# Kernel optimization log

Hardware: AMD Instinct MI355X
Metric: run time of the kernel (lower is better)

Reference implementation:

```python
import jax, jax.numpy as jnp
import numpy as np

N, E, B, C, L, HLS = 30000, 480000, 64, 128, 3, 64
PARAM_NAMES = ['Wq','bq','Wk','bk','Wv','bv','Wskip','bskip','lstm_Wih_f','lstm_Whh_f','lstm_bih_f','lstm_bhh_f','lstm_Wih_b','lstm_Whh_b','lstm_bih_b','lstm_bhh_b','att_W','att_b','gP_W1','gP_b1','gP_W2','gP_b2','gT_W1','gT_b1','gT_W2','gT_b2','m_W0','m_b0','m_W1','m_b1','m_W2','m_b2']


def setup_inputs() -> dict:
    key = jax.random.key(0)
    ks = iter(jax.random.split(key, 64))
    rn = lambda shape: jax.random.normal(next(ks), shape, dtype=jnp.float32) * 0.05
    inp = {
        'x': jax.random.normal(next(ks), (N, C), dtype=jnp.float32),
        'edge_index': jax.random.randint(next(ks), (2, E), 0, N, dtype=jnp.int32),
        'batch': jnp.sort(jax.random.randint(next(ks), (N,), 0, B, dtype=jnp.int32)),
        'hls_attr': jax.random.normal(next(ks), (B, HLS), dtype=jnp.float32),
        'Wq': rn((L, C, C)), 'bq': rn((L, C)),
        'Wk': rn((L, C, C)), 'bk': rn((L, C)),
        'Wv': rn((L, C, C)), 'bv': rn((L, C)),
        'Wskip': rn((L, C, C)), 'bskip': rn((L, C)),
        'lstm_Wih_f': rn((4 * C, C)), 'lstm_Whh_f': rn((4 * C, C)),
        'lstm_bih_f': rn((4 * C,)), 'lstm_bhh_f': rn((4 * C,)),
        'lstm_Wih_b': rn((4 * C, C)), 'lstm_Whh_b': rn((4 * C, C)),
        'lstm_bih_b': rn((4 * C,)), 'lstm_bhh_b': rn((4 * C,)),
        'att_W': rn((2 * C, 1)), 'att_b': rn((1,)),
        'gP_W1': rn((C, C)), 'gP_b1': rn((C,)), 'gP_W2': rn((C, 1)), 'gP_b2': rn((1,)),
        'gT_W1': rn((C, C)), 'gT_b1': rn((C,)), 'gT_W2': rn((C, 1)), 'gT_b2': rn((1,)),
        'm_W0': rn((2 * C + HLS, 64)), 'm_b0': rn((64,)),
        'm_W1': rn((64, 64)), 'm_b1': rn((64,)),
        'm_W2': rn((64, 1)), 'm_b2': rn((1,)),
    }
    return inp


def _segment_softmax(logits, seg, num):
    m = jax.ops.segment_max(logits, seg, num_segments=num)
    e = jnp.exp(logits - m[seg])
    d = jax.ops.segment_sum(e, seg, num_segments=num)
    return e / d[seg]


def _lstm(xs, Wih, Whh, bih, bhh):
    # xs: [L, N, C] -> outputs [L, N, H]
    H = Whh.shape[1]
    h0 = jnp.zeros((xs.shape[1], H), xs.dtype)
    bias = bih + bhh
    def step(carry, xt):
        h, c = carry
        z = xt @ Wih.T + h @ Whh.T + bias
        i, f, g, o = jnp.split(z, 4, axis=-1)
        c = jax.nn.sigmoid(f) * c + jax.nn.sigmoid(i) * jnp.tanh(g)
        h = jax.nn.sigmoid(o) * jnp.tanh(c)
        return (h, c), h
    _, hs = jax.lax.scan(step, (h0, h0), xs)
    return hs


def _gate_pool(x, batch, W1, b1, W2, b2):
    gate = jax.nn.relu(x @ W1 + b1) @ W2 + b2          # [N, 1]
    gate = _segment_softmax(gate[:, 0], batch, B)[:, None]
    return jax.ops.segment_sum(gate * x, batch, num_segments=B)


def _forward(x, edge_index, batch, hls_attr, Wq, bq, Wk, bk, Wv, bv, Wskip, bskip,
             lstm_Wih_f, lstm_Whh_f, lstm_bih_f, lstm_bhh_f,
             lstm_Wih_b, lstm_Whh_b, lstm_bih_b, lstm_bhh_b,
             att_W, att_b, gP_W1, gP_b1, gP_W2, gP_b2, gT_W1, gT_b1, gT_W2, gT_b2,
             m_W0, m_b0, m_W1, m_b1, m_W2, m_b2):
    src, dst = edge_index[0], edge_index[1]
    scale = 1.0 / jnp.sqrt(jnp.asarray(C, jnp.float32))
    h_list = []
    for i in range(L):
        q = x @ Wq[i] + bq[i]
        k = x @ Wk[i] + bk[i]
        v = x @ Wv[i] + bv[i]
        logits = jnp.sum(q[dst] * k[src], axis=-1) * scale   # [E]
        alpha = _segment_softmax(logits, dst, N)             # per-dst softmax
        agg = jax.ops.segment_sum(alpha[:, None] * v[src], dst, num_segments=N)
        x = jax.nn.relu(agg + x @ Wskip[i] + bskip[i])       # TransformerConv + root skip, then ReLU
        h_list.append(x)
    xs = jnp.stack(h_list)                                   # [L, N, C]
    hf = _lstm(xs, lstm_Wih_f, lstm_Whh_f, lstm_bih_f, lstm_bhh_f)
    hb = _lstm(xs[::-1], lstm_Wih_b, lstm_Whh_b, lstm_bih_b, lstm_bhh_b)[::-1]
    hcat = jnp.concatenate([hf, hb], axis=-1)                # [L, N, 2C]
    a = jax.nn.softmax((hcat @ att_W)[..., 0] + att_b[0], axis=0)  # softmax over layers
    x = jnp.sum(a[..., None] * xs, axis=0)                   # [N, C] JK-LSTM output
    out_P = _gate_pool(x, batch, gP_W1, gP_b1, gP_W2, gP_b2)
    out_T = _gate_pool(x, batch, gT_W1, gT_b1, gT_W2, gT_b2)
    h = jnp.concatenate([out_P, out_T, hls_attr], axis=-1)   # [B, 2C+HLS]
    h = jax.nn.relu(h @ m_W0 + m_b0)
    h = jax.nn.relu(h @ m_W1 + m_b1)
    return h @ m_W2 + m_b2                                   # [B, 1]


def reference(x, edge_index, batch, hls_attr, Wq, bq, Wk, bk, Wv, bv, Wskip, bskip,
              lstm_Wih_f, lstm_Whh_f, lstm_bih_f, lstm_bhh_f,
              lstm_Wih_b, lstm_Whh_b, lstm_bih_b, lstm_bhh_b,
              att_W, att_b, gP_W1, gP_b1, gP_W2, gP_b2, gT_W1, gT_b1, gT_W2, gT_b2,
              m_W0, m_b0, m_W1, m_b1, m_W2, m_b2):
    return _forward(x, edge_index, batch, hls_attr, Wq, bq, Wk, bk, Wv, bv, Wskip, bskip,
                    lstm_Wih_f, lstm_Whh_f, lstm_bih_f, lstm_bhh_f,
                    lstm_Wih_b, lstm_Whh_b, lstm_bih_b, lstm_bhh_b,
                    att_W, att_b, gP_W1, gP_b1, gP_W2, gP_b2, gT_W1, gT_b1, gT_W2, gT_b2,
                    m_W0, m_b0, m_W1, m_b1, m_W2, m_b2)
```

## Files before the change

### kernel.cpp

```cpp
#include <hip/hip_runtime.h>
#include <math.h>

#define NN 30000
#define EE 480000
#define BB 64
#define CC 128
#define LLAYERS 3
#define HLSD 64

typedef __attribute__((ext_vector_type(8))) short bf16x8;
typedef __attribute__((ext_vector_type(4))) float f32x4;

__device__ inline unsigned short f2bf(float f){
  unsigned u = __float_as_uint(f);
  u += 0x7fffu + ((u >> 16) & 1u);
  return (unsigned short)(u >> 16);
}
__device__ inline float bf2f(unsigned short h){
  return __uint_as_float(((unsigned)h) << 16);
}

__global__ void k_hist(const int* __restrict__ dst, int* __restrict__ counts, int E){
  int e = blockIdx.x*256 + threadIdx.x;
  if (e < E) atomicAdd(&counts[dst[e]], 1);
}
__global__ void k_scan_block(const int* __restrict__ counts, int* __restrict__ row_ptr,
                             int* __restrict__ bsums, int n){
  __shared__ int sm[256];
  int i = blockIdx.x*256 + threadIdx.x;
  int v = (i < n) ? counts[i] : 0;
  sm[threadIdx.x] = v; __syncthreads();
  for (int off = 1; off < 256; off <<= 1){
    int t = (threadIdx.x >= off) ? sm[threadIdx.x - off] : 0;
    __syncthreads();
    sm[threadIdx.x] += t;
    __syncthreads();
  }
  if (i < n) row_ptr[i+1] = sm[threadIdx.x];
  if (threadIdx.x == 255) bsums[blockIdx.x] = sm[255];
}
__global__ void k_scan_bsums(const int* __restrict__ bsums, int* __restrict__ bexcl, int nb){
  if (threadIdx.x == 0 && blockIdx.x == 0){
    int s = 0;
    for (int i = 0; i < nb; i++){ int t = bsums[i]; bexcl[i] = s; s += t; }
  }
}
__global__ void k_scan_add(int* __restrict__ row_ptr, const int* __restrict__ bexcl, int n){
  int i = blockIdx.x*256 + threadIdx.x;
  if (i < n) row_ptr[i+1] += bexcl[i >> 8];
  if (i == 0) row_ptr[0] = 0;
}
__global__ void k_fill(const int* __restrict__ src, const int* __restrict__ dst,
                       const int* __restrict__ row_ptr, int* __restrict__ fill,
                       int* __restrict__ esrc, int E){
  int e = blockIdx.x*256 + threadIdx.x;
  if (e < E){
    int d = dst[e];
    int pos = row_ptr[d] + atomicAdd(&fill[d], 1);
    esrc[pos] = src[e];
  }
}

struct PrepPtrs {
  const float* tsrc[14]; unsigned short* tdst[14];
  const float* csrc[4];  unsigned short* cdst[4];
  const float *bihf, *bhhf, *bihb, *bhhb;
  float *cbf, *cbb;
};
__global__ __launch_bounds__(256) void k_prep(PrepPtrs p){
  int b = blockIdx.x, tid = threadIdx.x;
  if (b < 14){
    const float* s = p.tsrc[b]; unsigned short* d = p.tdst[b];
    for (int i = tid; i < 16384; i += 256){
      int k = i >> 7, n = i & 127;
      d[n*128 + k] = f2bf(s[i]);
    }
  } else if (b < 30){
    int m = (b - 14) >> 2, ch = (b - 14) & 3;
    const float* s = p.csrc[m] + ch*16384; unsigned short* d = p.cdst[m] + ch*16384;
    for (int i = tid; i < 16384; i += 256) d[i] = f2bf(s[i]);
  } else {
    for (int i = tid; i < 512; i += 256){
      p.cbf[i] = p.bihf[i] + p.bhhf[i];
      p.cbb[i] = p.bihb[i] + p.bhhb[i];
    }
  }
}
__global__ __launch_bounds__(256) void k_cvt_x(const float* __restrict__ src,
                                               unsigned short* __restrict__ dst, int n8){
  int i = blockIdx.x*256 + threadIdx.x;
  if (i >= n8) return;
  float4 a = *(const float4*)(src + (size_t)i*8);
  float4 b = *(const float4*)(src + (size_t)i*8 + 4);
  union { unsigned short u[8]; uint4 v; } o;
  o.u[0]=f2bf(a.x); o.u[1]=f2bf(a.y); o.u[2]=f2bf(a.z); o.u[3]=f2bf(a.w);
  o.u[4]=f2bf(b.x); o.u[5]=f2bf(b.y); o.u[6]=f2bf(b.z); o.u[7]=f2bf(b.w);
  *(uint4*)(dst + (size_t)i*8) = o.v;
}

struct Quad { const unsigned short* Bt[4]; const float* bias[4]; };

template<int RELU, int OUTBF16>
__global__ __launch_bounds__(256) void k_mfma_gemm(
    const unsigned short* __restrict__ A0, Quad qd,
    float* __restrict__ Cf, unsigned short* __restrict__ Cb,
    int M, int ldC, int colsPerMat)
{
  __shared__ unsigned short As0[64*128];
  __shared__ unsigned short Bs0[64*128];

  const int tid = threadIdx.x;
  const int row0 = blockIdx.x*64;
  const int colg0 = blockIdx.y*64;
  const int mi = colg0 / colsPerMat;
  const int nloc = colg0 - mi*colsPerMat;
  const unsigned short* Bt0 = qd.Bt[mi];

  #pragma unroll
  for (int i = 0; i < 4; i++){
    int ch = tid + i*256;
    int r = ch >> 4, c16 = ch & 15;
    int gr = row0 + r;
    uint4 av = make_uint4(0,0,0,0);
    if (gr < M) av = *(const uint4*)(A0 + (size_t)gr*128 + c16*8);
    *(uint4*)((char*)As0 + ((r*256 + c16*16) ^ ((r&7)<<4))) = av;
    uint4 bv = *(const uint4*)(Bt0 + (size_t)(nloc + r)*128 + c16*8);
    *(uint4*)((char*)Bs0 + ((r*256 + c16*16) ^ ((r&7)<<4))) = bv;
  }
  __syncthreads();

  const int w = tid >> 6, l = tid & 63;
  const int lr = l & 15, lhi = l >> 4;

  f32x4 acc[4];
  #pragma unroll
  for (int f = 0; f < 4; f++){ acc[f][0]=0.f; acc[f][1]=0.f; acc[f][2]=0.f; acc[f][3]=0.f; }

  #pragma unroll
  for (int kt = 0; kt < 4; kt++){
    int arow = w*16 + lr;
    bf16x8 a = *(const bf16x8*)((const char*)As0 + ((arow*256 + kt*64 + lhi*16) ^ ((arow&7)<<4)));
    #pragma unroll
    for (int f = 0; f < 4; f++){
      int brow = f*16 + lr;
      bf16x8 b = *(const bf16x8*)((const char*)Bs0 + ((brow*256 + kt*64 + lhi*16) ^ ((brow&7)<<4)));
      acc[f] = __builtin_amdgcn_mfma_f32_16x16x32_bf16(a, b, acc[f], 0, 0, 0);
    }
  }

  const float* bias = qd.bias[mi];
  #pragma unroll
  for (int f = 0; f < 4; f++){
    int colg = colg0 + f*16 + lr;
    float bv = bias ? bias[nloc + f*16 + lr] : 0.f;
    #pragma unroll
    for (int r = 0; r < 4; r++){
      int grow = row0 + w*16 + lhi*4 + r;
      if (grow < M){
        float v = acc[f][r] + bv;
        if (RELU) v = fmaxf(v, 0.f);
        if (OUTBF16) Cb[(size_t)grow*ldC + colg] = f2bf(v);
        else         Cf[(size_t)grow*ldC + colg] = v;
      }
    }
  }
}

template<int FIRST>
__global__ __launch_bounds__(256) void k_lstm_fused(
    const unsigned short* __restrict__ X,
    const unsigned short* __restrict__ H,
    const unsigned short* __restrict__ Wih,
    const unsigned short* __restrict__ Whh,
    const float* __restrict__ cbias,
    unsigned short* __restrict__ Hout,
    float* __restrict__ Cst,
    float* __restrict__ score,
    const float* __restrict__ attW,
    int M)
{
  __shared__ unsigned short As[64*128];
  __shared__ unsigned short Bs[128*128];
  const int tid = threadIdx.x;
  const int row0 = blockIdx.x*64;
  const int t0 = blockIdx.y*32;
  const int w = tid >> 6, l = tid & 63, lr = l & 15, lhi = l >> 4;

  f32x4 acc[8];
  #pragma unroll
  for (int f = 0; f < 8; f++){ acc[f][0]=0.f; acc[f][1]=0.f; acc[f][2]=0.f; acc[f][3]=0.f; }

  const int npair = FIRST ? 1 : 2;
  for (int pair = 0; pair < npair; pair++){
    const unsigned short* A  = pair ? H   : X;
    const unsigned short* Bt = pair ? Whh : Wih;
    if (pair) __syncthreads();
    #pragma unroll
    for (int i = 0; i < 4; i++){
      int ch = tid + i*256;
      int r = ch >> 4, c16 = ch & 15;
      int gr = row0 + r;
      uint4 av = make_uint4(0,0,0,0);
      if (gr < M) av = *(const uint4*)(A + (size_t)gr*128 + c16*8);
      *(uint4*)((char*)As + ((r*256 + c16*16) ^ ((r&7)<<4))) = av;
    }
    #pragma unroll
    for (int i = 0; i < 8; i++){
      int ch = tid + i*256;
      int r = ch >> 4, c16 = ch & 15;
      int gr = (r >> 5)*128 + t0 + (r & 31);
      uint4 bv = *(const uint4*)(Bt + (size_t)gr*128 + c16*8);
      *(uint4*)((char*)Bs + ((r*256 + c16*16) ^ ((r&7)<<4))) = bv;
    }
    __syncthreads();
    #pragma unroll
    for (int kt = 0; kt < 4; kt++){
      int arow = w*16 + lr;
      bf16x8 a = *(const bf16x8*)((const char*)As + ((arow*256 + kt*64 + lhi*16) ^ ((arow&7)<<4)));
      #pragma unroll
      for (int f = 0; f < 8; f++){
        int brow = f*16 + lr;
        bf16x8 b = *(const bf16x8*)((const char*)Bs + ((brow*256 + kt*64 + lhi*16) ^ ((brow&7)<<4)));
        acc[f] = __builtin_amdgcn_mfma_f32_16x16x32_bf16(a, b, acc[f], 0, 0, 0);
      }
    }
  }

  float sc[4] = {0.f, 0.f, 0.f, 0.f};
  #pragma unroll
  for (int cb = 0; cb < 2; cb++){
    int t = t0 + cb*16 + lr;
    float aw  = attW[t];
    float bi  = cbias[t];
    float bf_ = cbias[128 + t];
    float bg  = cbias[256 + t];
    float bo  = cbias[384 + t];
    #pragma unroll
    for (int r = 0; r < 4; r++){
      int grow = row0 + w*16 + lhi*4 + r;
      if (grow < M){
        float zi = acc[0+cb][r] + bi;
        float zf = acc[2+cb][r] + bf_;
        float zg = acc[4+cb][r] + bg;
        float zo = acc[6+cb][r] + bo;
        float cp = FIRST ? 0.f : Cst[(size_t)grow*128 + t];
        float si = 1.f/(1.f + expf(-zi));
        float sf = 1.f/(1.f + expf(-zf));
        float so = 1.f/(1.f + expf(-zo));
        float cn = sf*cp + si*tanhf(zg);
        float hn = so*tanhf(cn);
        Cst[(size_t)grow*128 + t] = cn;
        Hout[(size_t)grow*128 + t] = f2bf(hn);
        sc[r] += hn * aw;
      }
    }
  }
  #pragma unroll
  for (int r = 0; r < 4; r++){
    float p = sc[r];
    p += __shfl_xor(p, 1, 64);
    p += __shfl_xor(p, 2, 64);
    p += __shfl_xor(p, 4, 64);
    p += __shfl_xor(p, 8, 64);
    if (lr == 0){
      int grow = row0 + w*16 + lhi*4 + r;
      if (grow < M) atomicAdd(&score[grow], p);
    }
  }
}

__global__ __launch_bounds__(256) void k_attn(
    const unsigned short* __restrict__ qkvs, const int* __restrict__ row_ptr,
    const int* __restrict__ esrc, unsigned short* __restrict__ xout, int n)
{
  int wid = threadIdx.x >> 6, lane = threadIdx.x & 63;
  int dst = blockIdx.x*4 + wid;
  if (dst >= n) return;
  const int g = lane >> 4, j = lane & 15;
  const size_t drow = (size_t)dst*512;

  bf16x8 qv = *(const bf16x8*)(qkvs + drow + j*8);
  float qf[8];
  #pragma unroll
  for (int i = 0; i < 8; i++) qf[i] = bf2f((unsigned short)qv[i]);

  const int rs = row_ptr[dst], re = row_ptr[dst+1];
  const float scale2 = 0.08838834764831845f * 1.4426950408889634f;
  float m = -INFINITY, den = 0.f;
  float acc[8];
  #pragma unroll
  for (int i = 0; i < 8; i++) acc[i] = 0.f;

  int e = rs + g;
  if (e < re){
    int s = esrc[e];
    const unsigned short* sr = qkvs + (size_t)s*512 + j*8;
    bf16x8 kc = *(const bf16x8*)(sr + 128);
    bf16x8 vc = *(const bf16x8*)(sr + 256);
    while (true){
      int en = e + 4;
      bool havenext = en < re;
      bf16x8 kn, vn;
      if (havenext){
        int sn = esrc[en];
        const unsigned short* srn = qkvs + (size_t)sn*512 + j*8;
        kn = *(const bf16x8*)(srn + 128);
        vn = *(const bf16x8*)(srn + 256);
      }
      float d = qf[0]*bf2f((unsigned short)kc[0]);
      #pragma unroll
      for (int i = 1; i < 8; i++) d += qf[i]*bf2f((unsigned short)kc[i]);
      d += __shfl_xor(d, 1, 64);
      d += __shfl_xor(d, 2, 64);
      d += __shfl_xor(d, 4, 64);
      d += __shfl_xor(d, 8, 64);
      float logit = d * scale2;
      float mn = fmaxf(m, logit);
      float rr = exp2f(m - mn);
      float wgt = exp2f(logit - mn);
      den = den*rr + wgt;
      #pragma unroll
      for (int i = 0; i < 8; i++)
        acc[i] = acc[i]*rr + wgt*bf2f((unsigned short)vc[i]);
      m = mn;
      if (!havenext) break;
      e = en; kc = kn; vc = vn;
    }
  }

  #pragma unroll
  for (int o = 16; o <= 32; o <<= 1){
    float mo  = __shfl_xor(m, o, 64);
    float dno = __shfl_xor(den, o, 64);
    float mn  = fmaxf(m, mo);
    float ss  = (m  > -INFINITY) ? exp2f(m  - mn) : 0.f;
    float so  = (mo > -INFINITY) ? exp2f(mo - mn) : 0.f;
    den = den*ss + dno*so;
    #pragma unroll
    for (int i = 0; i < 8; i++){
      float ao = __shfl_xor(acc[i], o, 64);
      acc[i] = acc[i]*ss + ao*so;
    }
    m = mn;
  }

  if (g == 0){
    bf16x8 sk = *(const bf16x8*)(qkvs + drow + 384 + j*8);
    float inv = (re > rs) ? 1.f/den : 0.f;
    union { unsigned short u[8]; uint4 v; } o8;
    #pragma unroll
    for (int i = 0; i < 8; i++){
      float v = acc[i]*inv + bf2f((unsigned short)sk[i]);
      o8.u[i] = f2bf(fmaxf(v, 0.f));
    }
    *(uint4*)(xout + (size_t)dst*128 + j*8) = o8.v;
  }
}

__global__ void k_jk_weights(const float* __restrict__ sF, const float* __restrict__ sB,
                             const float* __restrict__ attb, float* __restrict__ a, int n){
  int i = blockIdx.x*256 + threadIdx.x;
  if (i >= n) return;
  float s0 = sF[i]       + sB[i]       + attb[0];
  float s1 = sF[n+i]     + sB[n+i]     + attb[0];
  float s2 = sF[2*n+i]   + sB[2*n+i]   + attb[0];
  float mm = fmaxf(s0, fmaxf(s1, s2));
  float e0 = expf(s0-mm), e1 = expf(s1-mm), e2 = expf(s2-mm);
  float d = e0 + e1 + e2;
  a[i] = e0/d; a[n+i] = e1/d; a[2*n+i] = e2/d;
}
__global__ void k_jk_combine(const float* __restrict__ a,
                             const unsigned short* __restrict__ x0,
                             const unsigned short* __restrict__ x1,
                             const unsigned short* __restrict__ x2,
                             float* __restrict__ xjk, unsigned short* __restrict__ xjkb, int n){
  int idx = blockIdx.x*256 + threadIdx.x;
  if (idx >= n*128) return;
  int node = idx >> 7;
  float r = a[node]     * bf2f(x0[idx])
          + a[n+node]   * bf2f(x1[idx])
          + a[2*n+node] * bf2f(x2[idx]);
  xjk[idx] = r;
  xjkb[idx] = f2bf(r);
}

__global__ __launch_bounds__(256) void k_rowdot(const unsigned short* __restrict__ g,
                                                const float* __restrict__ w2,
                                                const float* __restrict__ b2, float* __restrict__ out, int n){
  int wid = threadIdx.x >> 6, lane = threadIdx.x & 63;
  int node = blockIdx.x*4 + wid;
  if (node >= n) return;
  ushort2 gv = *(const ushort2*)(g + (size_t)node*128 + lane*2);
  float2 wv = *(const float2*)(w2 + lane*2);
  float p = bf2f(gv.x)*wv.x + bf2f(gv.y)*wv.y;
  #pragma unroll
  for (int o = 1; o < 64; o <<= 1) p += __shfl_xor(p, o, 64);
  if (lane == 0) out[node] = p + b2[0];
}

__global__ void k_segbounds(const int* __restrict__ batch, int* __restrict__ segp, int n){
  int i = blockIdx.x*256 + threadIdx.x;
  if (i >= n) return;
  int b = batch[i];
  int bp = (i == 0) ? -1 : batch[i-1];
  for (int s = bp+1; s <= b; s++) segp[s] = i;
  if (i == n-1){
    for (int s = b+1; s <= BB; s++) segp[s] = n;
  }
}

__global__ __launch_bounds__(256) void k_seg_stats(
    const float* __restrict__ glP, const float* __restrict__ glT,
    const int* __restrict__ segp, float4* __restrict__ stats)
{
  const int b = blockIdx.x, tid = threadIdx.x;
  const int s0 = segp[b], s1 = segp[b+1];
  __shared__ float sred[8];

  float mP = -INFINITY, mT = -INFINITY;
  for (int i = s0 + tid; i < s1; i += 256){
    mP = fmaxf(mP, glP[i]);
    mT = fmaxf(mT, glT[i]);
  }
  #pragma unroll
  for (int o = 1; o < 64; o <<= 1){
    mP = fmaxf(mP, __shfl_xor(mP, o, 64));
    mT = fmaxf(mT, __shfl_xor(mT, o, 64));
  }
  if ((tid & 63) == 0){ sred[(tid >> 6)*2] = mP; sred[(tid >> 6)*2 + 1] = mT; }
  __syncthreads();
  mP = fmaxf(fmaxf(sred[0], sred[2]), fmaxf(sred[4], sred[6]));
  mT = fmaxf(fmaxf(sred[1], sred[3]), fmaxf(sred[5], sred[7]));
  __syncthreads();

  float dP = 0.f, dT = 0.f;
  for (int i = s0 + tid; i < s1; i += 256){
    dP += expf(glP[i] - mP);
    dT += expf(glT[i] - mT);
  }
  #pragma unroll
  for (int o = 1; o < 64; o <<= 1){
    dP += __shfl_xor(dP, o, 64);
    dT += __shfl_xor(dT, o, 64);
  }
  if ((tid & 63) == 0){ sred[(tid >> 6)*2] = dP; sred[(tid >> 6)*2 + 1] = dT; }
  __syncthreads();
  if (tid == 0){
    dP = sred[0] + sred[2] + sred[4] + sred[6];
    dT = sred[1] + sred[3] + sred[5] + sred[7];
    float4 st;
    st.x = mP; st.y = mT;
    st.z = (dP > 0.f) ? 1.f/dP : 0.f;
    st.w = (dT > 0.f) ? 1.f/dT : 0.f;
    stats[b] = st;
  }
}

__global__ __launch_bounds__(256) void k_poolsum(
    const float* __restrict__ xjk, const int* __restrict__ segp,
    const float* __restrict__ glP, const float* __restrict__ glT,
    const float4* __restrict__ stats,
    float* __restrict__ poolP, float* __restrict__ poolT)
{
  const int b = blockIdx.x;
  const int s0 = segp[b], s1 = segp[b+1];
  const float4 st = stats[b];
  const int half = threadIdx.x >> 7, c = threadIdx.x & 127;
  const int stream = blockIdx.y*2 + half;
  float aP = 0.f, aT = 0.f;
  for (int i = s0 + stream; i < s1; i += 32){
    float eP = expf(glP[i] - st.x);
    float eT = expf(glT[i] - st.y);
    float xv = xjk[(size_t)i*128 + c];
    aP += eP*xv; aT += eT*xv;
  }
  if (aP != 0.f) atomicAdd(&poolP[(size_t)b*128 + c], aP*st.z);
  if (aT != 0.f) atomicAdd(&poolT[(size_t)b*128 + c], aT*st.w);
}

__global__ __launch_bounds__(64) void k_mlp(
    const float* __restrict__ poolP, const float* __restrict__ poolT, const float* __restrict__ hls,
    const float* __restrict__ W0, const float* __restrict__ b0,
    const float* __restrict__ W1, const float* __restrict__ b1,
    const float* __restrict__ W2, const float* __restrict__ b2, float* __restrict__ out)
{
  __shared__ float hin[320];
  __shared__ float h1[64];
  int b = blockIdx.x, j = threadIdx.x;
  for (int i = j; i < 320; i += 64){
    float vv;
    if (i < 128)      vv = poolP[(size_t)b*128 + i];
    else if (i < 256) vv = poolT[(size_t)b*128 + (i-128)];
    else              vv = hls[(size_t)b*64 + (i-256)];
    hin[i] = vv;
  }
  __syncthreads();
  float s = b0[j];
  for (int kk = 0; kk < 320; kk++) s += hin[kk] * W0[kk*64 + j];
  h1[j] = fmaxf(s, 0.f);
  __syncthreads();
  float s2 = b1[j];
  for (int kk = 0; kk < 64; kk++) s2 += h1[kk] * W1[kk*64 + j];
  float h2 = fmaxf(s2, 0.f);
  float p = h2 * W2[j];
  #pragma unroll
  for (int o = 1; o < 64; o <<= 1) p += __shfl_xor(p, o, 64);
  if (j == 0) out[b] = p + b2[0];
}

extern "C" void kernel_launch(void* const* d_in, const int* in_sizes, int n_in,
                              void* d_out, int out_size, void* d_ws, size_t ws_size,
                              hipStream_t stream)
{
  (void)in_sizes; (void)n_in; (void)out_size; (void)ws_size;
  const int N = NN, E = EE, C = CC;
  const float* x     = (const float*)d_in[0];
  const int*   ei    = (const int*)d_in[1];
  const int*   batch = (const int*)d_in[2];
  const float* hls   = (const float*)d_in[3];
  const float* Wq = (const float*)d_in[4],  *bq = (const float*)d_in[5];
  const float* Wk = (const float*)d_in[6],  *bk = (const float*)d_in[7];
  const float* Wv = (const float*)d_in[8],  *bv = (const float*)d_in[9];
  const float* Ws = (const float*)d_in[10], *bs = (const float*)d_in[11];
  const float* Wih_f = (const float*)d_in[12], *Whh_f = (const float*)d_in[13];
  const float* bih_f = (const float*)d_in[14], *bhh_f = (const float*)d_in[15];
  const float* Wih_b = (const float*)d_in[16], *Whh_b = (const float*)d_in[17];
  const float* bih_b = (const float*)d_in[18], *bhh_b = (const float*)d_in[19];
  const float* attW  = (const float*)d_in[20], *attb  = (const float*)d_in[21];
  const float* gPW1 = (const float*)d_in[22], *gPb1 = (const float*)d_in[23];
  const float* gPW2 = (const float*)d_in[24], *gPb2 = (const float*)d_in[25];
  const float* gTW1 = (const float*)d_in[26], *gTb1 = (const float*)d_in[27];
  const float* gTW2 = (const float*)d_in[28], *gTb2 = (const float*)d_in[29];
  const float* mW0 = (const float*)d_in[30], *mb0 = (const float*)d_in[31];
  const float* mW1 = (const float*)d_in[32], *mb1 = (const float*)d_in[33];
  const float* mW2 = (const float*)d_in[34], *mb2 = (const float*)d_in[35];
  float* out = (float*)d_out;

  const int* esrc_in = ei;
  const int* edst_in = ei + E;

  typedef unsigned short u16;

  char* ws = (char*)d_ws;
  size_t off = 0;
  auto alloc = [&](size_t bytes) -> char* {
    char* p = ws + off;
    off += (bytes + 255) & ~(size_t)255;
    return p;
  };
  u16* qkvsb   = (u16*)alloc((size_t)N*512*2);
  u16* xb      = (u16*)alloc((size_t)N*C*2);
  u16* xsb0    = (u16*)alloc((size_t)N*C*2);
  u16* xsb1    = (u16*)alloc((size_t)N*C*2);
  u16* xsb2    = (u16*)alloc((size_t)N*C*2);
  u16* hbA     = (u16*)alloc((size_t)N*C*2);
  u16* hbB     = (u16*)alloc((size_t)N*C*2);
  float* cbuf  = (float*)alloc((size_t)N*C*4);
  float* scores= (float*)alloc((size_t)6*N*4);
  float* ajk   = (float*)alloc((size_t)3*N*4);
  float* xjk   = (float*)alloc((size_t)N*C*4);
  u16* xjkb    = (u16*)alloc((size_t)N*C*2);
  u16* g1P     = (u16*)alloc((size_t)N*C*2);
  u16* g1T     = (u16*)alloc((size_t)N*C*2);
  int* counts  = (int*)alloc((size_t)N*4);
  int* row_ptr = (int*)alloc((size_t)(N+1)*4);
  int* bsums   = (int*)alloc(512);
  int* bexcl   = (int*)alloc(512);
  int* esrc    = (int*)alloc((size_t)E*4);
  float* glP   = (float*)alloc((size_t)N*4);
  float* glT   = (float*)alloc((size_t)N*4);
  int* segp    = (int*)alloc((size_t)(BB+1)*4);
  float* poolP = (float*)alloc((size_t)BB*C*4);
  float* poolT = (float*)alloc((size_t)BB*C*4);
  float4* sstats = (float4*)alloc((size_t)BB*16);
  u16* wT      = (u16*)alloc((size_t)14*16384*2);
  u16* wLSTM   = (u16*)alloc((size_t)4*65536*2);
  float* combF = (float*)alloc(512*4);
  float* combB = (float*)alloc(512*4);

  float* scF = scores;
  float* scB = scores + (size_t)3*N;

  u16* wTq = wT;
  u16* wTk = wT + 3*16384;
  u16* wTv = wT + 6*16384;
  u16* wTs = wT + 9*16384;
  u16* wTgP = wT + 12*16384;
  u16* wTgT = wT + 13*16384;
  u16* wIHf = wLSTM;
  u16* wHHf = wLSTM + 65536;
  u16* wIHb = wLSTM + 2*65536;
  u16* wHHb = wLSTM + 3*65536;

  const int NB  = (N + 255)/256;
  const int EBL = (E + 255)/256;

  PrepPtrs pp;
  for (int l = 0; l < 3; l++){
    pp.tsrc[l]   = Wq + (size_t)l*16384;  pp.tdst[l]   = wTq + (size_t)l*16384;
    pp.tsrc[3+l] = Wk + (size_t)l*16384;  pp.tdst[3+l] = wTk + (size_t)l*16384;
    pp.tsrc[6+l] = Wv + (size_t)l*16384;  pp.tdst[6+l] = wTv + (size_t)l*16384;
    pp.tsrc[9+l] = Ws + (size_t)l*16384;  pp.tdst[9+l] = wTs + (size_t)l*16384;
  }
  pp.tsrc[12] = gPW1; pp.tdst[12] = wTgP;
  pp.tsrc[13] = gTW1; pp.tdst[13] = wTgT;
  pp.csrc[0] = Wih_f; pp.cdst[0] = wIHf;
  pp.csrc[1] = Whh_f; pp.cdst[1] = wHHf;
  pp.csrc[2] = Wih_b; pp.cdst[2] = wIHb;
  pp.csrc[3] = Whh_b; pp.cdst[3] = wHHb;
  pp.bihf = bih_f; pp.bhhf = bhh_f; pp.bihb = bih_b; pp.bhhb = bhh_b;
  pp.cbf = combF; pp.cbb = combB;
  k_prep<<<31, 256, 0, stream>>>(pp);
  k_cvt_x<<<(N*C/8 + 255)/256, 256, 0, stream>>>(x, xb, N*C/8);

  hipMemsetAsync(counts, 0, (size_t)N*4, stream);
  k_hist<<<EBL, 256, 0, stream>>>(edst_in, counts, E);
  k_scan_block<<<NB, 256, 0, stream>>>(counts, row_ptr, bsums, N);
  k_scan_bsums<<<1, 64, 0, stream>>>(bsums, bexcl, NB);
  k_scan_add<<<NB, 256, 0, stream>>>(row_ptr, bexcl, N);
  hipMemsetAsync(counts, 0, (size_t)N*4, stream);
  k_fill<<<EBL, 256, 0, stream>>>(esrc_in, edst_in, row_ptr, counts, esrc, E);

  const int GX = (N + 63)/64;
  dim3 blk(256);

  u16* xsb[3] = {xsb0, xsb1, xsb2};
  const u16* ain = xb;
  for (int l = 0; l < LLAYERS; l++){
    Quad q;
    q.Bt[0] = wTq + (size_t)l*16384;  q.bias[0] = bq + (size_t)l*C;
    q.Bt[1] = wTk + (size_t)l*16384;  q.bias[1] = bk + (size_t)l*C;
    q.Bt[2] = wTv + (size_t)l*16384;  q.bias[2] = bv + (size_t)l*C;
    q.Bt[3] = wTs + (size_t)l*16384;  q.bias[3] = bs + (size_t)l*C;
    k_mfma_gemm<0,1><<<dim3(GX,8), blk, 0, stream>>>(ain, q, nullptr, qkvsb, N, 512, 128);
    k_attn<<<(N+3)/4, 256, 0, stream>>>(qkvsb, row_ptr, esrc, xsb[l], N);
    ain = xsb[l];
  }

  hipMemsetAsync(scores, 0, (size_t)6*N*4, stream);
  {
    u16* hbuf2[2] = {hbA, hbB};
    for (int t = 0; t < 3; t++){
      u16* hout = hbuf2[t & 1];
      u16* hin2 = hbuf2[(t & 1) ^ 1];
      if (t == 0)
        k_lstm_fused<1><<<dim3(GX,4), blk, 0, stream>>>(xsb[t], nullptr, wIHf, nullptr, combF,
                                                        hout, cbuf, scF + (size_t)t*N, attW, N);
      else
        k_lstm_fused<0><<<dim3(GX,4), blk, 0, stream>>>(xsb[t], hin2, wIHf, wHHf, combF,
                                                        hout, cbuf, scF + (size_t)t*N, attW, N);
    }
    for (int s = 0; s < 3; s++){
      int t = 2 - s;
      u16* hout = hbuf2[s & 1];
      u16* hin2 = hbuf2[(s & 1) ^ 1];
      if (s == 0)
        k_lstm_fused<1><<<dim3(GX,4), blk, 0, stream>>>(xsb[t], nullptr, wIHb, nullptr, combB,
                                                        hout, cbuf, scB + (size_t)t*N, attW + 128, N);
      else
        k_lstm_fused<0><<<dim3(GX,4), blk, 0, stream>>>(xsb[t], hin2, wIHb, wHHb, combB,
                                                        hout, cbuf, scB + (size_t)t*N, attW + 128, N);
    }
  }

  k_jk_weights<<<NB, 256, 0, stream>>>(scF, scB, attb, ajk, N);
  k_jk_combine<<<(N*C + 255)/256, 256, 0, stream>>>(ajk, xsb0, xsb1, xsb2, xjk, xjkb, N);

  {
    Quad qp; qp.Bt[0]=wTgP; qp.bias[0]=gPb1; qp.Bt[1]=nullptr; qp.bias[1]=nullptr; qp.Bt[2]=nullptr; qp.bias[2]=nullptr; qp.Bt[3]=nullptr; qp.bias[3]=nullptr;
    k_mfma_gemm<1,1><<<dim3(GX,2), blk, 0, stream>>>(xjkb, qp, nullptr, g1P, N, 128, 128);
    k_rowdot<<<(N+3)/4, 256, 0, stream>>>(g1P, gPW2, gPb2, glP, N);
    Quad qt; qt.Bt[0]=wTgT; qt.bias[0]=gTb1; qt.Bt[1]=nullptr; qt.bias[1]=nullptr; qt.Bt[2]=nullptr; qt.bias[2]=nullptr; qt.Bt[3]=nullptr; qt.bias[3]=nullptr;
    k_mfma_gemm<1,1><<<dim3(GX,2), blk, 0, stream>>>(xjkb, qt, nullptr, g1T, N, 128, 128);
    k_rowdot<<<(N+3)/4, 256, 0, stream>>>(g1T, gTW2, gTb2, glT, N);
  }

  k_segbounds<<<NB, 256, 0, stream>>>(batch, segp, N);
  k_seg_stats<<<BB, 256, 0, stream>>>(glP, glT, segp, sstats);
  hipMemsetAsync(poolP, 0, (size_t)2*BB*C*4, stream);
  k_poolsum<<<dim3(BB,16), 256, 0, stream>>>(xjk, segp, glP, glT, sstats, poolP, poolT);

  k_mlp<<<BB, 64, 0, stream>>>(poolP, poolT, hls, mW0, mb0, mW1, mb1, mW2, mb2, out);
}
```

Before: 524.5 us.

## Merge LSTM directions per launch, fuse gate GEMMs, vectorize JK combine, fast math

The forward and backward LSTM steps now run in a single launch per time step, with the grid's y dimension doubled and the direction chosen by blockIdx.y. Each direction gets its own hidden and cell buffers. The two gate-pool first-layer GEMMs become one GEMM with 256 output columns, followed by one row-dot kernel that produces both logits. The JK combine kernel is vectorized to 8 elements per thread, and sigmoid, tanh and exp switch to fast intrinsics, trading some accuracy for fewer kernel launches and less ALU and memory traffic.

New measurement: 472.3 us. 10.0% less time.

```diff
diff --git a/kernel.cpp b/kernel.cpp
--- a/kernel.cpp
+++ b/kernel.cpp
@@ -10,6 +10,7 @@
 
 typedef __attribute__((ext_vector_type(8))) short bf16x8;
 typedef __attribute__((ext_vector_type(4))) float f32x4;
+typedef unsigned short u16;
 
 __device__ inline unsigned short f2bf(float f){
   unsigned u = __float_as_uint(f);
@@ -18,6 +19,12 @@
 }
 __device__ inline float bf2f(unsigned short h){
   return __uint_as_float(((unsigned)h) << 16);
+}
+__device__ inline float fsig(float z){
+  return __builtin_amdgcn_rcpf(1.f + __expf(-z));
+}
+__device__ inline float ftanh(float z){
+  return 1.f - 2.f*__builtin_amdgcn_rcpf(1.f + __expf(2.f*z));
 }
 
 __global__ void k_hist(const int* __restrict__ dst, int* __restrict__ counts, int E){
@@ -166,24 +173,35 @@
   }
 }
 
+struct LstmArgs {
+  const u16 *Xf, *Xb, *Hf, *Hb;
+  const u16 *Wihf, *Whhf, *Wihb, *Whhb;
+  const float *cbf, *cbb;
+  u16 *Hof, *Hob;
+  float *Cf, *Cb2;
+  float *scF, *scB;
+  const float* attW;
+  int M;
+};
 template<int FIRST>
-__global__ __launch_bounds__(256) void k_lstm_fused(
-    const unsigned short* __restrict__ X,
-    const unsigned short* __restrict__ H,
-    const unsigned short* __restrict__ Wih,
-    const unsigned short* __restrict__ Whh,
-    const float* __restrict__ cbias,
-    unsigned short* __restrict__ Hout,
-    float* __restrict__ Cst,
-    float* __restrict__ score,
-    const float* __restrict__ attW,
-    int M)
-{
+__global__ __launch_bounds__(256) void k_lstm2(LstmArgs a){
   __shared__ unsigned short As[64*128];
   __shared__ unsigned short Bs[128*128];
+  const int dir = blockIdx.y >> 2;
+  const int t0 = (blockIdx.y & 3)*32;
+  const u16* X = dir ? a.Xb : a.Xf;
+  const u16* H = dir ? a.Hb : a.Hf;
+  const u16* Wih = dir ? a.Wihb : a.Wihf;
+  const u16* Whh = dir ? a.Whhb : a.Whhf;
+  const float* cbias = dir ? a.cbb : a.cbf;
+  u16* Hout = dir ? a.Hob : a.Hof;
+  float* Cst = dir ? a.Cb2 : a.Cf;
+  float* score = dir ? a.scB : a.scF;
+  const float* attW = a.attW + dir*128;
+  const int M = a.M;
+
   const int tid = threadIdx.x;
   const int row0 = blockIdx.x*64;
-  const int t0 = blockIdx.y*32;
   const int w = tid >> 6, l = tid & 63, lr = l & 15, lhi = l >> 4;
 
   f32x4 acc[8];
@@ -216,12 +234,12 @@
     #pragma unroll
     for (int kt = 0; kt < 4; kt++){
       int arow = w*16 + lr;
-      bf16x8 a = *(const bf16x8*)((const char*)As + ((arow*256 + kt*64 + lhi*16) ^ ((arow&7)<<4)));
+      bf16x8 av = *(const bf16x8*)((const char*)As + ((arow*256 + kt*64 + lhi*16) ^ ((arow&7)<<4)));
       #pragma unroll
       for (int f = 0; f < 8; f++){
         int brow = f*16 + lr;
-        bf16x8 b = *(const bf16x8*)((const char*)Bs + ((brow*256 + kt*64 + lhi*16) ^ ((brow&7)<<4)));
-        acc[f] = __builtin_amdgcn_mfma_f32_16x16x32_bf16(a, b, acc[f], 0, 0, 0);
+        bf16x8 bv = *(const bf16x8*)((const char*)Bs + ((brow*256 + kt*64 + lhi*16) ^ ((brow&7)<<4)));
+        acc[f] = __builtin_amdgcn_mfma_f32_16x16x32_bf16(av, bv, acc[f], 0, 0, 0);
       }
     }
   }
@@ -244,11 +262,8 @@
         float zg = acc[4+cb][r] + bg;
         float zo = acc[6+cb][r] + bo;
         float cp = FIRST ? 0.f : Cst[(size_t)grow*128 + t];
-        float si = 1.f/(1.f + expf(-zi));
-        float sf = 1.f/(1.f + expf(-zf));
-        float so = 1.f/(1.f + expf(-zo));
-        float cn = sf*cp + si*tanhf(zg);
-        float hn = so*tanhf(cn);
+        float cn = fsig(zf)*cp + fsig(zi)*ftanh(zg);
+        float hn = fsig(zo)*ftanh(cn);
         Cst[(size_t)grow*128 + t] = cn;
         Hout[(size_t)grow*128 + t] = f2bf(hn);
         sc[r] += hn * aw;
@@ -365,7 +380,7 @@
   float s1 = sF[n+i]     + sB[n+i]     + attb[0];
   float s2 = sF[2*n+i]   + sB[2*n+i]   + attb[0];
   float mm = fmaxf(s0, fmaxf(s1, s2));
-  float e0 = expf(s0-mm), e1 = expf(s1-mm), e2 = expf(s2-mm);
+  float e0 = __expf(s0-mm), e1 = __expf(s1-mm), e2 = __expf(s2-mm);
   float d = e0 + e1 + e2;
   a[i] = e0/d; a[n+i] = e1/d; a[2*n+i] = e2/d;
 }
@@ -374,28 +389,44 @@
                              const unsigned short* __restrict__ x1,
                              const unsigned short* __restrict__ x2,
                              float* __restrict__ xjk, unsigned short* __restrict__ xjkb, int n){
-  int idx = blockIdx.x*256 + threadIdx.x;
-  if (idx >= n*128) return;
-  int node = idx >> 7;
-  float r = a[node]     * bf2f(x0[idx])
-          + a[n+node]   * bf2f(x1[idx])
-          + a[2*n+node] * bf2f(x2[idx]);
-  xjk[idx] = r;
-  xjkb[idx] = f2bf(r);
-}
-
-__global__ __launch_bounds__(256) void k_rowdot(const unsigned short* __restrict__ g,
-                                                const float* __restrict__ w2,
-                                                const float* __restrict__ b2, float* __restrict__ out, int n){
+  int i8 = blockIdx.x*256 + threadIdx.x;
+  if (i8 >= n*16) return;
+  int node = i8 >> 4;
+  float a0 = a[node], a1 = a[n+node], a2 = a[2*n+node];
+  bf16x8 v0 = *(const bf16x8*)(x0 + (size_t)i8*8);
+  bf16x8 v1 = *(const bf16x8*)(x1 + (size_t)i8*8);
+  bf16x8 v2 = *(const bf16x8*)(x2 + (size_t)i8*8);
+  float r[8];
+  union { unsigned short u[8]; uint4 v; } ob;
+  #pragma unroll
+  for (int i = 0; i < 8; i++){
+    r[i] = a0*bf2f((unsigned short)v0[i]) + a1*bf2f((unsigned short)v1[i]) + a2*bf2f((unsigned short)v2[i]);
+    ob.u[i] = f2bf(r[i]);
+  }
+  float4* xo = (float4*)(xjk + (size_t)i8*8);
+  xo[0] = make_float4(r[0], r[1], r[2], r[3]);
+  xo[1] = make_float4(r[4], r[5], r[6], r[7]);
+  *(uint4*)(xjkb + (size_t)i8*8) = ob.v;
+}
+
+__global__ __launch_bounds__(256) void k_rowdot2(
+    const unsigned short* __restrict__ g,
+    const float* __restrict__ w2P, const float* __restrict__ w2T,
+    const float* __restrict__ b2P, const float* __restrict__ b2T,
+    float* __restrict__ glP, float* __restrict__ glT, int n)
+{
   int wid = threadIdx.x >> 6, lane = threadIdx.x & 63;
   int node = blockIdx.x*4 + wid;
   if (node >= n) return;
-  ushort2 gv = *(const ushort2*)(g + (size_t)node*128 + lane*2);
-  float2 wv = *(const float2*)(w2 + lane*2);
-  float p = bf2f(gv.x)*wv.x + bf2f(gv.y)*wv.y;
-  #pragma unroll
-  for (int o = 1; o < 64; o <<= 1) p += __shfl_xor(p, o, 64);
-  if (lane == 0) out[node] = p + b2[0];
+  ushort4 gv = *(const ushort4*)(g + (size_t)node*256 + lane*4);
+  const float* w = (lane >= 32) ? w2T : w2P;
+  int c0 = (lane*4) & 127;
+  float4 wv = *(const float4*)(w + c0);
+  float p = bf2f(gv.x)*wv.x + bf2f(gv.y)*wv.y + bf2f(gv.z)*wv.z + bf2f(gv.w)*wv.w;
+  #pragma unroll
+  for (int o = 1; o < 32; o <<= 1) p += __shfl_xor(p, o, 64);
+  if (lane == 0)  glP[node] = p + b2P[0];
+  if (lane == 32) glT[node] = p + b2T[0];
 }
 
 __global__ void k_segbounds(const int* __restrict__ batch, int* __restrict__ segp, int n){
@@ -435,8 +466,8 @@
 
   float dP = 0.f, dT = 0.f;
   for (int i = s0 + tid; i < s1; i += 256){
-    dP += expf(glP[i] - mP);
-    dT += expf(glT[i] - mT);
+    dP += __expf(glP[i] - mP);
+    dT += __expf(glT[i] - mT);
   }
   #pragma unroll
   for (int o = 1; o < 64; o <<= 1){
@@ -469,8 +500,8 @@
   const int stream = blockIdx.y*2 + half;
   float aP = 0.f, aT = 0.f;
   for (int i = s0 + stream; i < s1; i += 32){
-    float eP = expf(glP[i] - st.x);
-    float eT = expf(glT[i] - st.y);
+    float eP = __expf(glP[i] - st.x);
+    float eT = __expf(glT[i] - st.y);
     float xv = xjk[(size_t)i*128 + c];
     aP += eP*xv; aT += eT*xv;
   }
@@ -539,8 +570,6 @@
   const int* esrc_in = ei;
   const int* edst_in = ei + E;
 
-  typedef unsigned short u16;
-
   char* ws = (char*)d_ws;
   size_t off = 0;
   auto alloc = [&](size_t bytes) -> char* {
@@ -553,15 +582,17 @@
   u16* xsb0    = (u16*)alloc((size_t)N*C*2);
   u16* xsb1    = (u16*)alloc((size_t)N*C*2);
   u16* xsb2    = (u16*)alloc((size_t)N*C*2);
+  u16* hfA     = (u16*)alloc((size_t)N*C*2);
+  u16* hfB     = (u16*)alloc((size_t)N*C*2);
   u16* hbA     = (u16*)alloc((size_t)N*C*2);
   u16* hbB     = (u16*)alloc((size_t)N*C*2);
-  float* cbuf  = (float*)alloc((size_t)N*C*4);
+  float* cfb   = (float*)alloc((size_t)N*C*4);
+  float* cbb2  = (float*)alloc((size_t)N*C*4);
   float* scores= (float*)alloc((size_t)6*N*4);
   float* ajk   = (float*)alloc((size_t)3*N*4);
   float* xjk   = (float*)alloc((size_t)N*C*4);
   u16* xjkb    = (u16*)alloc((size_t)N*C*2);
-  u16* g1P     = (u16*)alloc((size_t)N*C*2);
-  u16* g1T     = (u16*)alloc((size_t)N*C*2);
+  u16* g1PT    = (u16*)alloc((size_t)N*256*2);
   int* counts  = (int*)alloc((size_t)N*4);
   int* row_ptr = (int*)alloc((size_t)(N+1)*4);
   int* bsums   = (int*)alloc(512);
@@ -639,40 +670,34 @@
 
   hipMemsetAsync(scores, 0, (size_t)6*N*4, stream);
   {
-    u16* hbuf2[2] = {hbA, hbB};
-    for (int t = 0; t < 3; t++){
-      u16* hout = hbuf2[t & 1];
-      u16* hin2 = hbuf2[(t & 1) ^ 1];
-      if (t == 0)
-        k_lstm_fused<1><<<dim3(GX,4), blk, 0, stream>>>(xsb[t], nullptr, wIHf, nullptr, combF,
-                                                        hout, cbuf, scF + (size_t)t*N, attW, N);
-      else
-        k_lstm_fused<0><<<dim3(GX,4), blk, 0, stream>>>(xsb[t], hin2, wIHf, wHHf, combF,
-                                                        hout, cbuf, scF + (size_t)t*N, attW, N);
-    }
-    for (int s = 0; s < 3; s++){
-      int t = 2 - s;
-      u16* hout = hbuf2[s & 1];
-      u16* hin2 = hbuf2[(s & 1) ^ 1];
-      if (s == 0)
-        k_lstm_fused<1><<<dim3(GX,4), blk, 0, stream>>>(xsb[t], nullptr, wIHb, nullptr, combB,
-                                                        hout, cbuf, scB + (size_t)t*N, attW + 128, N);
-      else
-        k_lstm_fused<0><<<dim3(GX,4), blk, 0, stream>>>(xsb[t], hin2, wIHb, wHHb, combB,
-                                                        hout, cbuf, scB + (size_t)t*N, attW + 128, N);
+    u16* hfbuf[2] = {hfA, hfB};
+    u16* hbbuf[2] = {hbA, hbB};
+    for (int step = 0; step < 3; step++){
+      LstmArgs la;
+      la.Xf = xsb[step]; la.Xb = xsb[2-step];
+      la.Hf = hfbuf[(step&1)^1]; la.Hb = hbbuf[(step&1)^1];
+      la.Wihf = wIHf; la.Whhf = wHHf; la.Wihb = wIHb; la.Whhb = wHHb;
+      la.cbf = combF; la.cbb = combB;
+      la.Hof = hfbuf[step&1]; la.Hob = hbbuf[step&1];
+      la.Cf = cfb; la.Cb2 = cbb2;
+      la.scF = scF + (size_t)step*N; la.scB = scB + (size_t)(2-step)*N;
+      la.attW = attW; la.M = N;
+      if (step == 0) k_lstm2<1><<<dim3(GX,8), blk, 0, stream>>>(la);
+      else           k_lstm2<0><<<dim3(GX,8), blk, 0, stream>>>(la);
     }
   }
 
   k_jk_weights<<<NB, 256, 0, stream>>>(scF, scB, attb, ajk, N);
-  k_jk_combine<<<(N*C + 255)/256, 256, 0, stream>>>(ajk, xsb0, xsb1, xsb2, xjk, xjkb, N);
+  k_jk_combine<<<(N*16 + 255)/256, 256, 0, stream>>>(ajk, xsb0, xsb1, xsb2, xjk, xjkb, N);
 
   {
-    Quad qp; qp.Bt[0]=wTgP; qp.bias[0]=gPb1; qp.Bt[1]=nullptr; qp.bias[1]=nullptr; qp.Bt[2]=nullptr; qp.bias[2]=nullptr; qp.Bt[3]=nullptr; qp.bias[3]=nullptr;
-    k_mfma_gemm<1,1><<<dim3(GX,2), blk, 0, stream>>>(xjkb, qp, nullptr, g1P, N, 128, 128);
-    k_rowdot<<<(N+3)/4, 256, 0, stream>>>(g1P, gPW2, gPb2, glP, N);
-    Quad qt; qt.Bt[0]=wTgT; qt.bias[0]=gTb1; qt.Bt[1]=nullptr; qt.bias[1]=nullptr; qt.Bt[2]=nullptr; qt.bias[2]=nullptr; qt.Bt[3]=nullptr; qt.bias[3]=nullptr;
-    k_mfma_gemm<1,1><<<dim3(GX,2), blk, 0, stream>>>(xjkb, qt, nullptr, g1T, N, 128, 128);
-    k_rowdot<<<(N+3)/4, 256, 0, stream>>>(g1T, gTW2, gTb2, glT, N);
+    Quad qg;
+    qg.Bt[0] = wTgP; qg.bias[0] = gPb1;
+    qg.Bt[1] = wTgT; qg.bias[1] = gTb1;
+    qg.Bt[2] = nullptr; qg.bias[2] = nullptr;
+    qg.Bt[3] = nullptr; qg.bias[3] = nullptr;
+    k_mfma_gemm<1,1><<<dim3(GX,4), blk, 0, stream>>>(xjkb, qg, nullptr, g1PT, N, 256, 128);
+    k_rowdot2<<<(N+3)/4, 256, 0, stream>>>(g1PT, gPW2, gTW2, gPb2, gTb2, glP, glT, N);
   }
 
   k_segbounds<<<NB, 256, 0, stream>>>(batch, segp, N);
```
